# Optimization experiments

Measured on AMD Instinct MI355X. Metric: run time of the kernel, lower is better.

Reference implementation:

```python
import jax, jax.numpy as jnp
import numpy as np

D_LATENT, D_HIDDEN, D_TIME, K = 128, 256, 16, 3
B, NX = 8, 4096
MSG_IN = 2 * D_LATENT + 1 + D_TIME + 2  # 275
UPD_IN = 2 * D_LATENT + D_TIME          # 272


def _gelu(v):
    return jax.nn.gelu(v, approximate=False)  # torch nn.GELU default (erf)


def _linear_params(key, din, dout):
    k1, k2 = jax.random.split(key)
    bound = 1.0 / np.sqrt(din)
    w = jax.random.uniform(k1, (din, dout), minval=-bound, maxval=bound, dtype=jnp.float32)
    b = jax.random.uniform(k2, (dout,), minval=-bound, maxval=bound, dtype=jnp.float32)
    return w, b


def setup_inputs() -> dict:
    key = jax.random.key(0)
    ks = jax.random.split(key, 16)
    inp = {
        'h': jax.random.normal(ks[0], (B, NX, D_LATENT), dtype=jnp.float32),
        'x': jax.random.uniform(ks[1], (B, NX), dtype=jnp.float32),
        'tau': jax.random.normal(ks[2], (B, D_TIME), dtype=jnp.float32),
        'u0': jax.random.normal(ks[3], (B, NX), dtype=jnp.float32),
    }
    inp['msg_w1'], inp['msg_b1'] = _linear_params(ks[4], MSG_IN, D_HIDDEN)
    inp['msg_w2'], inp['msg_b2'] = _linear_params(ks[5], D_HIDDEN, D_HIDDEN)
    inp['msg_w3'], inp['msg_b3'] = _linear_params(ks[6], D_HIDDEN, D_LATENT)
    inp['gate_w1'], inp['gate_b1'] = _linear_params(ks[7], MSG_IN, D_HIDDEN)
    inp['gate_w2'], inp['gate_b2'] = _linear_params(ks[8], D_HIDDEN, 1)
    inp['upd_w1'], inp['upd_b1'] = _linear_params(ks[9], UPD_IN, D_HIDDEN)
    inp['upd_w2'], inp['upd_b2'] = _linear_params(ks[10], D_HIDDEN, D_HIDDEN)
    inp['upd_w3'], inp['upd_b3'] = _linear_params(ks[11], D_HIDDEN, D_LATENT)
    inp['W_w'], inp['W_b'] = _linear_params(ks[12], D_LATENT, D_LATENT)
    return inp


def reference(h, x, tau, u0, msg_w1, msg_b1, msg_w2, msg_b2, msg_w3, msg_b3,
              gate_w1, gate_b1, gate_w2, gate_b2,
              upd_w1, upd_b1, upd_w2, upd_b2, upd_w3, upd_b3, W_w, W_b):
    Bq, nx, d = h.shape
    k = K
    S = 2 * k + 1
    # replicate padding along the spatial dim
    h_pad = jnp.pad(h, ((0, 0), (k, k), (0, 0)), mode='edge')
    x_pad = jnp.pad(x, ((0, 0), (k, k)), mode='edge')
    u0_pad = jnp.pad(u0, ((0, 0), (k, k)), mode='edge')
    # all stencil windows at once: idx[nx, S] gathers neighbor j for node i
    idx = jnp.arange(nx)[:, None] + jnp.arange(S)[None, :]
    h_j = h_pad[:, idx, :]                                  # [B, nx, S, d]
    rel = (x_pad[:, idx] - x[:, :, None])[..., None]        # [B, nx, S, 1]
    du0 = (u0[:, :, None] - u0_pad[:, idx])[..., None]      # [B, nx, S, 1]
    h_e = jnp.broadcast_to(h[:, :, None, :], (Bq, nx, S, d))
    tau_e = jnp.broadcast_to(tau[:, None, None, :], (Bq, nx, S, tau.shape[-1]))
    msg_in = jnp.concatenate([h_e, h_j, rel, tau_e, du0, jnp.abs(du0)], axis=-1)  # [B,nx,S,275]
    a = _gelu(msg_in @ msg_w1 + msg_b1)
    a = _gelu(a @ msg_w2 + msg_b2)
    msg = a @ msg_w3 + msg_b3                               # [B, nx, S, d]
    g = _gelu(msg_in @ gate_w1 + gate_b1)
    gate = jax.nn.sigmoid(g @ gate_w2 + gate_b2)            # [B, nx, S, 1]
    agg = jnp.sum(gate * msg, axis=2)                       # [B, nx, d]
    tau_n = jnp.broadcast_to(tau[:, None, :], (Bq, nx, tau.shape[-1]))
    upd_in = jnp.concatenate([h, agg, tau_n], axis=-1)      # [B, nx, 272]
    u = _gelu(upd_in @ upd_w1 + upd_b1)
    u = _gelu(u @ upd_w2 + upd_b2)
    h_nonlocal = u @ upd_w3 + upd_b3
    h_local = h @ W_w + W_b
    return _gelu(h_nonlocal + h_local)
```

## Files before the change

kernel.cpp:

```cpp
#include <hip/hip_runtime.h>
#include <hip/hip_bf16.h>
#include <math.h>

#define NXC 4096
#define NNODES 32768

typedef __attribute__((ext_vector_type(8))) short bf16x8;
typedef __attribute__((ext_vector_type(4))) short s16x4;
typedef __attribute__((ext_vector_type(16))) float f32x16;

#define MFMA32(a,b,c) __builtin_amdgcn_mfma_f32_32x32x16_bf16((a),(b),(c),0,0,0)

__device__ __forceinline__ float gelu_f(float v) {
    float z = v * fmaf(v*v, 0.10294324f, 2.3022082f);
    float e = __builtin_amdgcn_exp2f(z);
    return v - v * __builtin_amdgcn_rcpf(1.0f + e);
}
__device__ __forceinline__ float sigmoid_f(float v) {
    float e = __builtin_amdgcn_exp2f(-1.4426950409f * v);
    return __builtin_amdgcn_rcpf(1.0f + e);
}
__device__ __forceinline__ short f2bs(float x) {
    __hip_bfloat16 b = __float2bfloat16(x);
    union { __hip_bfloat16 h; short s; } u; u.h = b; return u.s;
}
__device__ __forceinline__ f32x16 zero16() {
    f32x16 v;
    #pragma unroll
    for (int i = 0; i < 16; ++i) v[i] = 0.f;
    return v;
}
__device__ __forceinline__ float dpp_xor1(float x) {
    return __int_as_float(__builtin_amdgcn_update_dpp(0, __float_as_int(x), 0xB1, 0xF, 0xF, true));
}
__device__ __forceinline__ float dpp_xor2(float x) {
    return __int_as_float(__builtin_amdgcn_update_dpp(0, __float_as_int(x), 0x4E, 0xF, 0xF, true));
}

__global__ void tau_kernel(const float* __restrict__ tau,
                           const float* __restrict__ msg_w1, const float* __restrict__ msg_b1,
                           const float* __restrict__ gate_w1, const float* __restrict__ gate_b1,
                           const float* __restrict__ upd_w1, const float* __restrict__ upd_b1,
                           float* __restrict__ TM, float* __restrict__ TG, float* __restrict__ TU)
{
    const int b = blockIdx.x;
    const int t = threadIdx.x;
    float tv[16];
    #pragma unroll
    for (int k = 0; k < 16; ++k) tv[k] = tau[b*16 + k];
    float am = msg_b1[t], ag = gate_b1[t], au = upd_b1[t];
    #pragma unroll
    for (int k = 0; k < 16; ++k) {
        am = fmaf(tv[k], msg_w1 [(257+k)*256 + t], am);
        ag = fmaf(tv[k], gate_w1[(257+k)*256 + t], ag);
        au = fmaf(tv[k], upd_w1 [(256+k)*256 + t], au);
    }
    TM[b*256+t] = am; TG[b*256+t] = ag; TU[b*256+t] = au;
}

__global__ void wconv_kernel(const float* __restrict__ msg_w2, const float* __restrict__ msg_w3,
                             const float* __restrict__ msg_w1, const float* __restrict__ gate_w1,
                             const float* __restrict__ upd_w1, const float* __restrict__ upd_w2,
                             const float* __restrict__ upd_w3, const float* __restrict__ W_w,
                             __hip_bfloat16* __restrict__ w2t, __hip_bfloat16* __restrict__ w3t,
                             __hip_bfloat16* __restrict__ wall_t, __hip_bfloat16* __restrict__ w1ut,
                             __hip_bfloat16* __restrict__ w2ut, __hip_bfloat16* __restrict__ w3ut,
                             __hip_bfloat16* __restrict__ wwt)
{
    int i = blockIdx.x * 256 + threadIdx.x;
    if (i < 65536) { int c=i>>8, k=i&255; w2t[i] = __float2bfloat16(msg_w2[k*256+c]); return; }
    i -= 65536;
    if (i < 32768) { int c=i>>8, k=i&255; w3t[i] = __float2bfloat16(msg_w3[k*128+c]); return; }
    i -= 32768;
    if (i < 131072) {
        int c = i>>7, k = i&127; float v;
        if      (c <  256) v = msg_w1 [k*256 + c];
        else if (c <  512) v = msg_w1 [(128+k)*256 + (c-256)];
        else if (c <  768) v = gate_w1[k*256 + (c-512)];
        else               v = gate_w1[(128+k)*256 + (c-768)];
        wall_t[i] = __float2bfloat16(v); return;
    }
    i -= 131072;
    if (i < 65536) { int c=i>>8, k=i&255; w1ut[i] = __float2bfloat16(upd_w1[k*256+c]); return; }
    i -= 65536;
    if (i < 65536) { int c=i>>8, k=i&255; w2ut[i] = __float2bfloat16(upd_w2[k*256+c]); return; }
    i -= 65536;
    if (i < 32768) { int c=i>>8, k=i&255; w3ut[i] = __float2bfloat16(upd_w3[k*128+c]); return; }
    i -= 32768;
    { int c=i>>7, k=i&127; wwt[i] = __float2bfloat16(W_w[k*128+c]); }
}

#define PSTR 136

__global__ __launch_bounds__(256, 4)
void precompute_kernel(const float* __restrict__ h, const __hip_bfloat16* __restrict__ wall_t,
                       __hip_bfloat16* __restrict__ PAm, __hip_bfloat16* __restrict__ PBm,
                       __hip_bfloat16* __restrict__ PAg, __hip_bfloat16* __restrict__ PBg)
{
    __shared__ __align__(16) __hip_bfloat16 lds[64*256];
    const int t = threadIdx.x;
    const int lane = t & 63, wv = t >> 6;
    const int cl = lane & 31, g = lane >> 5;
    const int base = blockIdx.x * 64;
    const int tile = blockIdx.y;

    #pragma unroll
    for (int i = 0; i < 8; ++i) {
        int f = (i*256 + t)*4;
        float4 hv = *(const float4*)&h[(size_t)base*128 + f];
        int row = f >> 7, col = f & 127;
        s16x4 pk; pk[0]=f2bs(hv.x); pk[1]=f2bs(hv.y); pk[2]=f2bs(hv.z); pk[3]=f2bs(hv.w);
        *(s16x4*)&lds[row*PSTR + col] = pk;
    }
    __syncthreads();

    f32x16 a00 = zero16(), a01 = zero16(), a10 = zero16(), a11 = zero16();
    {
        const int c0 = wv*64 + cl, c1 = c0 + 32;
        const __hip_bfloat16* b0 = wall_t + ((size_t)tile*256 + c0)*128 + g*8;
        const __hip_bfloat16* b1 = wall_t + ((size_t)tile*256 + c1)*128 + g*8;
        const __hip_bfloat16* a0 = lds + (size_t)(cl)*PSTR + g*8;
        const __hip_bfloat16* a1p = lds + (size_t)(32+cl)*PSTR + g*8;
        #pragma unroll
        for (int kt = 0; kt < 8; ++kt) {
            bf16x8 bf0 = *(const bf16x8*)(b0 + kt*16);
            bf16x8 bf1 = *(const bf16x8*)(b1 + kt*16);
            bf16x8 af0 = *(const bf16x8*)(a0 + kt*16);
            bf16x8 af1 = *(const bf16x8*)(a1p + kt*16);
            a00 = MFMA32(af0, bf0, a00);
            a01 = MFMA32(af0, bf1, a01);
            a10 = MFMA32(af1, bf0, a10);
            a11 = MFMA32(af1, bf1, a11);
        }
    }
    __syncthreads();
    {
        const int c0 = wv*64 + cl, c1 = c0 + 32;
        #pragma unroll
        for (int r = 0; r < 16; ++r) {
            int row = (r&3) + 8*(r>>2) + 4*g;
            lds[row*256 + c0]      = __float2bfloat16(a00[r]);
            lds[row*256 + c1]      = __float2bfloat16(a01[r]);
            lds[(32+row)*256 + c0] = __float2bfloat16(a10[r]);
            lds[(32+row)*256 + c1] = __float2bfloat16(a11[r]);
        }
    }
    __syncthreads();
    {
        __hip_bfloat16* bufs[4] = {PAm, PBm, PAg, PBg};
        __hip_bfloat16* dst = bufs[tile];
        #pragma unroll
        for (int i = 0; i < 8; ++i) {
            int idx = i*256 + t;
            int row = idx >> 5, ch = idx & 31;
            *(float4*)&dst[(size_t)(base+row)*256 + ch*8] =
                *(const float4*)&lds[row*256 + ch*8];
        }
    }
}

#define ENPB 8
#define EEPB 56
#define ARS  264
#define MRS  132

__global__ __launch_bounds__(256, 4)
void edge_kernel(const float* __restrict__ x, const float* __restrict__ u0,
                 const float* __restrict__ msg_w1, const float* __restrict__ gate_w1,
                 const __hip_bfloat16* __restrict__ w2t, const float* __restrict__ msg_b2,
                 const __hip_bfloat16* __restrict__ w3t, const float* __restrict__ msg_b3,
                 const float* __restrict__ gate_w2, const float* __restrict__ gate_b2,
                 const __hip_bfloat16* __restrict__ PAm, const __hip_bfloat16* __restrict__ PBm,
                 const __hip_bfloat16* __restrict__ PAg, const __hip_bfloat16* __restrict__ PBg,
                 const float* __restrict__ TM, const float* __restrict__ TG,
                 float* __restrict__ AGG)
{
    __shared__ __align__(16) __hip_bfloat16 act[64*ARS];
    __shared__ float s_gp[4][EEPB];
    __shared__ float s_rel[EEPB], s_du[EEPB], s_ad[EEPB];
    __shared__ int   s_slotj[14];
    __shared__ float s_gate[EEPB];

    const int t    = threadIdx.x;
    const int lane = t & 63;
    const int wv   = t >> 6;
    const int base = blockIdx.x * ENPB;
    const int b    = base >> 12;
    const int ii0  = base & (NXC-1);

    if (t < 14) {
        int jj = ii0 - 3 + t;
        jj = jj < 0 ? 0 : (jj > NXC-1 ? NXC-1 : jj);
        s_slotj[t] = b*NXC + jj;
    }
    if (t < EEPB) {
        int nd = t / 7, s = t - nd*7;
        int i  = base + nd;
        int jj = ii0 + nd + s - 3;
        jj = jj < 0 ? 0 : (jj > NXC-1 ? NXC-1 : jj);
        int j = b*NXC + jj;
        float rel = x[j] - x[i];
        float du  = u0[i] - u0[j];
        s_rel[t] = rel; s_du[t] = du; s_ad[t] = fabsf(du);
    }
    __syncthreads();

    {
        float wr  = msg_w1 [256*256+t], wd  = msg_w1 [273*256+t], wa  = msg_w1 [274*256+t];
        float gwr = gate_w1[256*256+t], gwd = gate_w1[273*256+t], gwa = gate_w1[274*256+t];
        float tm = TM[b*256+t], tg = TG[b*256+t];
        float g2 = gate_w2[t];
        float bm[14], bg[14], pam[8], pag[8], sacc[14];
        #pragma unroll
        for (int q = 0; q < 14; ++q) {
            size_t o = (size_t)s_slotj[q]*256 + t;
            bm[q] = __bfloat162float(PBm[o]) + tm;
            bg[q] = __bfloat162float(PBg[o]) + tg;
        }
        #pragma unroll
        for (int nd = 0; nd < 8; ++nd) {
            size_t o = (size_t)(base+nd)*256 + t;
            pam[nd] = __bfloat162float(PAm[o]);
            pag[nd] = __bfloat162float(PAg[o]);
        }
        const bool p1 = (lane & 1), p2 = ((lane & 2) != 0);
        #pragma unroll
        for (int m = 0; m < 14; ++m) {
            float gq[4];
            #pragma unroll
            for (int r4i = 0; r4i < 4; ++r4i) {
                const int e = m*4 + r4i;
                const int nd = e / 7, s = e - nd*7, q = nd + s;
                float rel = s_rel[e], du = s_du[e], ad = s_ad[e];
                float pm = pam[nd] + bm[q];
                pm = fmaf(rel, wr, pm); pm = fmaf(du, wd, pm); pm = fmaf(ad, wa, pm);
                act[e*ARS + t] = __float2bfloat16(gelu_f(pm));
                float pg = pag[nd] + bg[q];
                pg = fmaf(rel, gwr, pg); pg = fmaf(du, gwd, pg); pg = fmaf(ad, gwa, pg);
                gq[r4i] = gelu_f(pg) * g2;
            }
            float xx = p1 ? gq[1] : gq[0], yy = p1 ? gq[0] : gq[1];
            xx += dpp_xor1(yy);
            float zz = p1 ? gq[3] : gq[2], ww = p1 ? gq[2] : gq[3];
            zz += dpp_xor1(ww);
            float uu = p2 ? zz : xx, vv = p2 ? xx : zz;
            uu += dpp_xor2(vv);
            sacc[m] = uu;
        }
        #pragma unroll
        for (int m = 0; m < 14; ++m) {
            float v = sacc[m];
            v += __shfl_xor(v, 4);
            v += __shfl_xor(v, 8);
            v += __shfl_xor(v, 16);
            v += __shfl_xor(v, 32);
            if (lane < 4) s_gp[wv][m*4 + lane] = v;
        }
    }
    __syncthreads();
    if (t < EEPB)
        s_gate[t] = sigmoid_f(s_gp[0][t] + s_gp[1][t] + s_gp[2][t] + s_gp[3][t] + gate_b2[0]);

    const int cl = lane & 31;
    const int g  = lane >> 5;
    f32x16 acc00 = zero16(), acc01 = zero16(), acc10 = zero16(), acc11 = zero16();
    {
        const __hip_bfloat16* w2a = w2t + (size_t)((wv*2+0)*32 + cl)*256 + g*8;
        const __hip_bfloat16* w2b = w2t + (size_t)((wv*2+1)*32 + cl)*256 + g*8;
        const __hip_bfloat16* a1a = act + (size_t)(cl)*ARS + g*8;
        const __hip_bfloat16* a1b = act + (size_t)(32+cl)*ARS + g*8;
        #pragma unroll
        for (int kt = 0; kt < 16; ++kt) {
            bf16x8 bfa = *(const bf16x8*)(w2a + kt*16);
            bf16x8 bfb = *(const bf16x8*)(w2b + kt*16);
            bf16x8 afa = *(const bf16x8*)(a1a + kt*16);
            bf16x8 afb = *(const bf16x8*)(a1b + kt*16);
            acc00 = MFMA32(afa, bfa, acc00);
            acc01 = MFMA32(afa, bfb, acc01);
            acc10 = MFMA32(afb, bfa, acc10);
            acc11 = MFMA32(afb, bfb, acc11);
        }
    }
    __syncthreads();
    {
        const int c0 = (wv*2+0)*32 + cl;
        const int c1 = (wv*2+1)*32 + cl;
        float b20 = msg_b2[c0], b21 = msg_b2[c1];
        #pragma unroll
        for (int r = 0; r < 16; ++r) {
            int row0 = (r&3) + 8*(r>>2) + 4*g;
            act[row0*ARS + c0] = __float2bfloat16(gelu_f(acc00[r] + b20));
            act[row0*ARS + c1] = __float2bfloat16(gelu_f(acc01[r] + b21));
            if (r < 12) {
                int row1 = 32 + row0;
                act[row1*ARS + c0] = __float2bfloat16(gelu_f(acc10[r] + b20));
                act[row1*ARS + c1] = __float2bfloat16(gelu_f(acc11[r] + b21));
            }
        }
    }
    __syncthreads();

    f32x16 m0 = zero16(), m1 = zero16();
    {
        const __hip_bfloat16* w3p = w3t + (size_t)(wv*32 + cl)*256 + g*8;
        const __hip_bfloat16* a2a = act + (size_t)(cl)*ARS + g*8;
        const __hip_bfloat16* a2b = act + (size_t)(32+cl)*ARS + g*8;
        #pragma unroll
        for (int kt = 0; kt < 16; ++kt) {
            bf16x8 bfr = *(const bf16x8*)(w3p + kt*16);
            m0 = MFMA32(*(const bf16x8*)(a2a + kt*16), bfr, m0);
            m1 = MFMA32(*(const bf16x8*)(a2b + kt*16), bfr, m1);
        }
    }
    __syncthreads();
    float* msgbuf = (float*)act;
    {
        const int c = wv*32 + cl;
        float b3v = msg_b3[c];
        #pragma unroll
        for (int r = 0; r < 16; ++r) {
            int row0 = (r&3) + 8*(r>>2) + 4*g;
            int row1 = 32 + row0;
            msgbuf[row0*MRS + c] = (m0[r] + b3v) * s_gate[row0];
            if (row1 < EEPB)
                msgbuf[row1*MRS + c] = (m1[r] + b3v) * s_gate[row1];
        }
    }
    __syncthreads();

    {
        const int c   = t & 127;
        const int grp = t >> 7;
        #pragma unroll
        for (int p = 0; p < 4; ++p) {
            int nd = grp + p*2;
            float ssum = 0.f;
            #pragma unroll
            for (int q2 = 0; q2 < 7; ++q2) ssum += msgbuf[(nd*7+q2)*MRS + c];
            AGG[(size_t)(base+nd)*128 + c] = ssum;
        }
    }
}

#define UM 32

__global__ __launch_bounds__(256, 4)
void update_kernel(const __hip_bfloat16* __restrict__ w1ut, const __hip_bfloat16* __restrict__ w2ut,
                   const __hip_bfloat16* __restrict__ w3ut, const __hip_bfloat16* __restrict__ wwt,
                   const float* __restrict__ upd_b2, const float* __restrict__ upd_b3,
                   const float* __restrict__ W_b,
                   const float* __restrict__ h, const float* __restrict__ AGG,
                   const float* __restrict__ TU,
                   float* __restrict__ out)
{
    __shared__ __align__(16) __hip_bfloat16 ub[UM*ARS];
    const int t = threadIdx.x;
    const int lane = t & 63, wv = t >> 6;
    const int cl = lane & 31, g = lane >> 5;
    const int base = blockIdx.x * UM;
    const int b = base >> 12;

    #pragma unroll
    for (int i = 0; i < 4; ++i) {
        int f = (i*256 + t)*4;
        int row = f >> 7, col = f & 127;
        float4 hv = *(const float4*)&h[(size_t)base*128 + f];
        s16x4 pk; pk[0]=f2bs(hv.x); pk[1]=f2bs(hv.y); pk[2]=f2bs(hv.z); pk[3]=f2bs(hv.w);
        *(s16x4*)&ub[row*ARS + col] = pk;
        float4 av = *(const float4*)&AGG[(size_t)base*128 + f];
        s16x4 pa; pa[0]=f2bs(av.x); pa[1]=f2bs(av.y); pa[2]=f2bs(av.z); pa[3]=f2bs(av.w);
        *(s16x4*)&ub[row*ARS + 128 + col] = pa;
    }
    __syncthreads();

    f32x16 u0a = zero16(), u1a = zero16(), hl = zero16();
    {
        const __hip_bfloat16* a0 = ub + (size_t)(cl)*ARS + g*8;
        const __hip_bfloat16* b0 = w1ut + (size_t)(wv*64 + cl)*256 + g*8;
        const __hip_bfloat16* b1 = w1ut + (size_t)(wv*64 + 32 + cl)*256 + g*8;
        const __hip_bfloat16* bw = wwt + (size_t)(wv*32 + cl)*128 + g*8;
        #pragma unroll
        for (int kt = 0; kt < 16; ++kt) {
            bf16x8 af = *(const bf16x8*)(a0 + kt*16);
            u0a = MFMA32(af, *(const bf16x8*)(b0 + kt*16), u0a);
            u1a = MFMA32(af, *(const bf16x8*)(b1 + kt*16), u1a);
            if (kt < 8)
                hl = MFMA32(af, *(const bf16x8*)(bw + kt*16), hl);
        }
    }
    __syncthreads();
    {
        const int c0 = wv*64 + cl, c1 = c0 + 32;
        float tu0 = TU[b*256 + c0], tu1 = TU[b*256 + c1];
        #pragma unroll
        for (int r = 0; r < 16; ++r) {
            int row = (r&3) + 8*(r>>2) + 4*g;
            ub[row*ARS + c0] = __float2bfloat16(gelu_f(u0a[r] + tu0));
            ub[row*ARS + c1] = __float2bfloat16(gelu_f(u1a[r] + tu1));
        }
    }
    __syncthreads();

    f32x16 v0a = zero16(), v1a = zero16();
    {
        const __hip_bfloat16* a0 = ub + (size_t)(cl)*ARS + g*8;
        const __hip_bfloat16* b0 = w2ut + (size_t)(wv*64 + cl)*256 + g*8;
        const __hip_bfloat16* b1 = w2ut + (size_t)(wv*64 + 32 + cl)*256 + g*8;
        #pragma unroll
        for (int kt = 0; kt < 16; ++kt) {
            bf16x8 af = *(const bf16x8*)(a0 + kt*16);
            v0a = MFMA32(af, *(const bf16x8*)(b0 + kt*16), v0a);
            v1a = MFMA32(af, *(const bf16x8*)(b1 + kt*16), v1a);
        }
    }
    __syncthreads();
    {
        const int c0 = wv*64 + cl, c1 = c0 + 32;
        float b20 = upd_b2[c0], b21 = upd_b2[c1];
        #pragma unroll
        for (int r = 0; r < 16; ++r) {
            int row = (r&3) + 8*(r>>2) + 4*g;
            ub[row*ARS + c0] = __float2bfloat16(gelu_f(v0a[r] + b20));
            ub[row*ARS + c1] = __float2bfloat16(gelu_f(v1a[r] + b21));
        }
    }
    __syncthreads();

    f32x16 w0a = zero16();
    {
        const __hip_bfloat16* wp = w3ut + (size_t)(wv*32 + cl)*256 + g*8;
        const __hip_bfloat16* a0 = ub + (size_t)(cl)*ARS + g*8;
        #pragma unroll
        for (int kt = 0; kt < 16; ++kt)
            w0a = MFMA32(*(const bf16x8*)(a0 + kt*16), *(const bf16x8*)(wp + kt*16), w0a);
    }
    {
        const int c = wv*32 + cl;
        float b3v = upd_b3[c] + W_b[c];
        #pragma unroll
        for (int r = 0; r < 16; ++r) {
            int row = (r&3) + 8*(r>>2) + 4*g;
            size_t o = (size_t)(base+row)*128 + c;
            out[o] = gelu_f(w0a[r] + b3v + hl[r]);
        }
    }
}

extern "C" void kernel_launch(void* const* d_in, const int* in_sizes, int n_in,
                              void* d_out, int out_size, void* d_ws, size_t ws_size,
                              hipStream_t stream)
{
    const float* h      = (const float*)d_in[0];
    const float* x      = (const float*)d_in[1];
    const float* tau    = (const float*)d_in[2];
    const float* u0     = (const float*)d_in[3];
    const float* msg_w1 = (const float*)d_in[4];
    const float* msg_b1 = (const float*)d_in[5];
    const float* msg_w2 = (const float*)d_in[6];
    const float* msg_b2 = (const float*)d_in[7];
    const float* msg_w3 = (const float*)d_in[8];
    const float* msg_b3 = (const float*)d_in[9];
    const float* gate_w1= (const float*)d_in[10];
    const float* gate_b1= (const float*)d_in[11];
    const float* gate_w2= (const float*)d_in[12];
    const float* gate_b2= (const float*)d_in[13];
    const float* upd_w1 = (const float*)d_in[14];
    const float* upd_b1 = (const float*)d_in[15];
    const float* upd_w2 = (const float*)d_in[16];
    const float* upd_b2 = (const float*)d_in[17];
    const float* upd_w3 = (const float*)d_in[18];
    const float* upd_b3 = (const float*)d_in[19];
    const float* W_w    = (const float*)d_in[20];
    const float* W_b    = (const float*)d_in[21];
    float* out = (float*)d_out;

    char* ws = (char*)d_ws;
    size_t off = 0;
    auto alloc = [&](size_t bytes) -> void* {
        void* p = ws + off;
        off += (bytes + 255) & ~(size_t)255;
        return p;
    };
    __hip_bfloat16* PAm = (__hip_bfloat16*)alloc((size_t)NNODES*256*2);
    __hip_bfloat16* PBm = (__hip_bfloat16*)alloc((size_t)NNODES*256*2);
    __hip_bfloat16* PAg = (__hip_bfloat16*)alloc((size_t)NNODES*256*2);
    __hip_bfloat16* PBg = (__hip_bfloat16*)alloc((size_t)NNODES*256*2);
    float* AGG = (float*)alloc((size_t)NNODES*128*4);
    float* TM  = (float*)alloc(8*256*4);
    float* TG  = (float*)alloc(8*256*4);
    float* TU  = (float*)alloc(8*256*4);
    __hip_bfloat16* w2t   = (__hip_bfloat16*)alloc((size_t)256*256*2);
    __hip_bfloat16* w3t   = (__hip_bfloat16*)alloc((size_t)128*256*2);
    __hip_bfloat16* wall_t= (__hip_bfloat16*)alloc((size_t)1024*128*2);
    __hip_bfloat16* w1ut  = (__hip_bfloat16*)alloc((size_t)256*256*2);
    __hip_bfloat16* w2ut  = (__hip_bfloat16*)alloc((size_t)256*256*2);
    __hip_bfloat16* w3ut  = (__hip_bfloat16*)alloc((size_t)128*256*2);
    __hip_bfloat16* wwt   = (__hip_bfloat16*)alloc((size_t)128*128*2);
    (void)ws_size; (void)in_sizes; (void)n_in; (void)out_size;

    tau_kernel<<<8, 256, 0, stream>>>(tau, msg_w1, msg_b1, gate_w1, gate_b1,
                                      upd_w1, upd_b1, TM, TG, TU);
    wconv_kernel<<<1600, 256, 0, stream>>>(msg_w2, msg_w3, msg_w1, gate_w1,
                                           upd_w1, upd_w2, upd_w3, W_w,
                                           w2t, w3t, wall_t, w1ut, w2ut, w3ut, wwt);
    precompute_kernel<<<dim3(NNODES/64, 4), 256, 0, stream>>>(h, wall_t,
                                                              PAm, PBm, PAg, PBg);
    edge_kernel<<<NNODES/ENPB, 256, 0, stream>>>(x, u0, msg_w1, gate_w1,
                                                 w2t, msg_b2, w3t, msg_b3,
                                                 gate_w2, gate_b2,
                                                 PAm, PBm, PAg, PBg, TM, TG, AGG);
    update_kernel<<<NNODES/UM, 256, 0, stream>>>(w1ut, w2ut, w3ut, wwt,
                                                 upd_b2, upd_b3, W_b,
                                                 h, AGG, TU, out);
}
```

Baseline: 205.0 us.

## Fuse tau into wconv, loop precompute tiles, pack GELU pairs, store AGG in bf16

Folds the tau projection kernel into the weight-conversion kernel as extra blocks, which removes one launch. The precompute kernel now loads h once per block and loops over all four output tiles, instead of using a 2D grid that reloads h for each tile. GELU and the elementwise math in the edge and update kernels are rewritten on 2-wide float vectors to allow packed FP32 instructions. AGG is stored as bf16, which halves its traffic and makes the update kernel's load a plain copy, at some precision cost in the intermediate. The trade-offs are fewer precompute blocks with more LDS each and extra barriers inside the tile loop.

```diff
diff --git a/kernel.cpp b/kernel.cpp
--- a/kernel.cpp
+++ b/kernel.cpp
@@ -8,6 +8,7 @@
 typedef __attribute__((ext_vector_type(8))) short bf16x8;
 typedef __attribute__((ext_vector_type(4))) short s16x4;
 typedef __attribute__((ext_vector_type(16))) float f32x16;
+typedef __attribute__((ext_vector_type(2))) float f32x2;
 
 #define MFMA32(a,b,c) __builtin_amdgcn_mfma_f32_32x32x16_bf16((a),(b),(c),0,0,0)
 
@@ -15,6 +16,15 @@
     float z = v * fmaf(v*v, 0.10294324f, 2.3022082f);
     float e = __builtin_amdgcn_exp2f(z);
     return v - v * __builtin_amdgcn_rcpf(1.0f + e);
+}
+__device__ __forceinline__ f32x2 gelu2(f32x2 v) {
+    const f32x2 c1 = {0.10294324f, 0.10294324f};
+    const f32x2 c2 = {2.3022082f, 2.3022082f};
+    f32x2 z = v * __builtin_elementwise_fma(v*v, c1, c2);
+    f32x2 r;
+    r[0] = __builtin_amdgcn_rcpf(1.0f + __builtin_amdgcn_exp2f(z[0]));
+    r[1] = __builtin_amdgcn_rcpf(1.0f + __builtin_amdgcn_exp2f(z[1]));
+    return v - v * r;
 }
 __device__ __forceinline__ float sigmoid_f(float v) {
     float e = __builtin_amdgcn_exp2f(-1.4426950409f * v);
@@ -37,36 +47,35 @@
     return __int_as_float(__builtin_amdgcn_update_dpp(0, __float_as_int(x), 0x4E, 0xF, 0xF, true));
 }
 
-__global__ void tau_kernel(const float* __restrict__ tau,
-                           const float* __restrict__ msg_w1, const float* __restrict__ msg_b1,
-                           const float* __restrict__ gate_w1, const float* __restrict__ gate_b1,
-                           const float* __restrict__ upd_w1, const float* __restrict__ upd_b1,
-                           float* __restrict__ TM, float* __restrict__ TG, float* __restrict__ TU)
-{
-    const int b = blockIdx.x;
-    const int t = threadIdx.x;
-    float tv[16];
-    #pragma unroll
-    for (int k = 0; k < 16; ++k) tv[k] = tau[b*16 + k];
-    float am = msg_b1[t], ag = gate_b1[t], au = upd_b1[t];
-    #pragma unroll
-    for (int k = 0; k < 16; ++k) {
-        am = fmaf(tv[k], msg_w1 [(257+k)*256 + t], am);
-        ag = fmaf(tv[k], gate_w1[(257+k)*256 + t], ag);
-        au = fmaf(tv[k], upd_w1 [(256+k)*256 + t], au);
-    }
-    TM[b*256+t] = am; TG[b*256+t] = ag; TU[b*256+t] = au;
-}
-
 __global__ void wconv_kernel(const float* __restrict__ msg_w2, const float* __restrict__ msg_w3,
                              const float* __restrict__ msg_w1, const float* __restrict__ gate_w1,
                              const float* __restrict__ upd_w1, const float* __restrict__ upd_w2,
                              const float* __restrict__ upd_w3, const float* __restrict__ W_w,
+                             const float* __restrict__ tau,
+                             const float* __restrict__ msg_b1, const float* __restrict__ gate_b1,
+                             const float* __restrict__ upd_b1,
                              __hip_bfloat16* __restrict__ w2t, __hip_bfloat16* __restrict__ w3t,
                              __hip_bfloat16* __restrict__ wall_t, __hip_bfloat16* __restrict__ w1ut,
                              __hip_bfloat16* __restrict__ w2ut, __hip_bfloat16* __restrict__ w3ut,
-                             __hip_bfloat16* __restrict__ wwt)
+                             __hip_bfloat16* __restrict__ wwt,
+                             float* __restrict__ TM, float* __restrict__ TG, float* __restrict__ TU)
 {
+    if (blockIdx.x >= 1600) {
+        const int b = blockIdx.x - 1600;
+        const int t = threadIdx.x;
+        float tv[16];
+        #pragma unroll
+        for (int k = 0; k < 16; ++k) tv[k] = tau[b*16 + k];
+        float am = msg_b1[t], ag = gate_b1[t], au = upd_b1[t];
+        #pragma unroll
+        for (int k = 0; k < 16; ++k) {
+            am = fmaf(tv[k], msg_w1 [(257+k)*256 + t], am);
+            ag = fmaf(tv[k], gate_w1[(257+k)*256 + t], ag);
+            au = fmaf(tv[k], upd_w1 [(256+k)*256 + t], au);
+        }
+        TM[b*256+t] = am; TG[b*256+t] = ag; TU[b*256+t] = au;
+        return;
+    }
     int i = blockIdx.x * 256 + threadIdx.x;
     if (i < 65536) { int c=i>>8, k=i&255; w2t[i] = __float2bfloat16(msg_w2[k*256+c]); return; }
     i -= 65536;
@@ -92,17 +101,17 @@
 
 #define PSTR 136
 
-__global__ __launch_bounds__(256, 4)
+__global__ __launch_bounds__(256, 3)
 void precompute_kernel(const float* __restrict__ h, const __hip_bfloat16* __restrict__ wall_t,
                        __hip_bfloat16* __restrict__ PAm, __hip_bfloat16* __restrict__ PBm,
                        __hip_bfloat16* __restrict__ PAg, __hip_bfloat16* __restrict__ PBg)
 {
-    __shared__ __align__(16) __hip_bfloat16 lds[64*256];
+    __shared__ __align__(16) __hip_bfloat16 hs[64*PSTR];
+    __shared__ __align__(16) __hip_bfloat16 ob[64*256];
     const int t = threadIdx.x;
     const int lane = t & 63, wv = t >> 6;
     const int cl = lane & 31, g = lane >> 5;
     const int base = blockIdx.x * 64;
-    const int tile = blockIdx.y;
 
     #pragma unroll
     for (int i = 0; i < 8; ++i) {
@@ -110,52 +119,50 @@
         float4 hv = *(const float4*)&h[(size_t)base*128 + f];
         int row = f >> 7, col = f & 127;
         s16x4 pk; pk[0]=f2bs(hv.x); pk[1]=f2bs(hv.y); pk[2]=f2bs(hv.z); pk[3]=f2bs(hv.w);
-        *(s16x4*)&lds[row*PSTR + col] = pk;
-    }
-    __syncthreads();
-
-    f32x16 a00 = zero16(), a01 = zero16(), a10 = zero16(), a11 = zero16();
-    {
-        const int c0 = wv*64 + cl, c1 = c0 + 32;
-        const __hip_bfloat16* b0 = wall_t + ((size_t)tile*256 + c0)*128 + g*8;
-        const __hip_bfloat16* b1 = wall_t + ((size_t)tile*256 + c1)*128 + g*8;
-        const __hip_bfloat16* a0 = lds + (size_t)(cl)*PSTR + g*8;
-        const __hip_bfloat16* a1p = lds + (size_t)(32+cl)*PSTR + g*8;
-        #pragma unroll
-        for (int kt = 0; kt < 8; ++kt) {
-            bf16x8 bf0 = *(const bf16x8*)(b0 + kt*16);
-            bf16x8 bf1 = *(const bf16x8*)(b1 + kt*16);
-            bf16x8 af0 = *(const bf16x8*)(a0 + kt*16);
-            bf16x8 af1 = *(const bf16x8*)(a1p + kt*16);
-            a00 = MFMA32(af0, bf0, a00);
-            a01 = MFMA32(af0, bf1, a01);
-            a10 = MFMA32(af1, bf0, a10);
-            a11 = MFMA32(af1, bf1, a11);
-        }
-    }
-    __syncthreads();
-    {
-        const int c0 = wv*64 + cl, c1 = c0 + 32;
+        *(s16x4*)&hs[row*PSTR + col] = pk;
+    }
+    __syncthreads();
+
+    __hip_bfloat16* bufs[4] = {PAm, PBm, PAg, PBg};
+    const int c0 = wv*64 + cl, c1 = c0 + 32;
+    const __hip_bfloat16* a0  = hs + (size_t)(cl)*PSTR + g*8;
+    const __hip_bfloat16* a1p = hs + (size_t)(32+cl)*PSTR + g*8;
+
+    for (int tile = 0; tile < 4; ++tile) {
+        f32x16 a00 = zero16(), a01 = zero16(), a10 = zero16(), a11 = zero16();
+        {
+            const __hip_bfloat16* b0 = wall_t + ((size_t)tile*256 + c0)*128 + g*8;
+            const __hip_bfloat16* b1 = wall_t + ((size_t)tile*256 + c1)*128 + g*8;
+            #pragma unroll
+            for (int kt = 0; kt < 8; ++kt) {
+                bf16x8 bf0 = *(const bf16x8*)(b0 + kt*16);
+                bf16x8 bf1 = *(const bf16x8*)(b1 + kt*16);
+                bf16x8 af0 = *(const bf16x8*)(a0 + kt*16);
+                bf16x8 af1 = *(const bf16x8*)(a1p + kt*16);
+                a00 = MFMA32(af0, bf0, a00);
+                a01 = MFMA32(af0, bf1, a01);
+                a10 = MFMA32(af1, bf0, a10);
+                a11 = MFMA32(af1, bf1, a11);
+            }
+        }
         #pragma unroll
         for (int r = 0; r < 16; ++r) {
             int row = (r&3) + 8*(r>>2) + 4*g;
-            lds[row*256 + c0]      = __float2bfloat16(a00[r]);
-            lds[row*256 + c1]      = __float2bfloat16(a01[r]);
-            lds[(32+row)*256 + c0] = __float2bfloat16(a10[r]);
-            lds[(32+row)*256 + c1] = __float2bfloat16(a11[r]);
-        }
-    }
-    __syncthreads();
-    {
-        __hip_bfloat16* bufs[4] = {PAm, PBm, PAg, PBg};
+            ob[row*256 + c0]      = __float2bfloat16(a00[r]);
+            ob[row*256 + c1]      = __float2bfloat16(a01[r]);
+            ob[(32+row)*256 + c0] = __float2bfloat16(a10[r]);
+            ob[(32+row)*256 + c1] = __float2bfloat16(a11[r]);
+        }
+        __syncthreads();
         __hip_bfloat16* dst = bufs[tile];
         #pragma unroll
         for (int i = 0; i < 8; ++i) {
             int idx = i*256 + t;
             int row = idx >> 5, ch = idx & 31;
             *(float4*)&dst[(size_t)(base+row)*256 + ch*8] =
-                *(const float4*)&lds[row*256 + ch*8];
-        }
+                *(const float4*)&ob[row*256 + ch*8];
+        }
+        __syncthreads();
     }
 }
 
@@ -173,11 +180,11 @@
                  const __hip_bfloat16* __restrict__ PAm, const __hip_bfloat16* __restrict__ PBm,
                  const __hip_bfloat16* __restrict__ PAg, const __hip_bfloat16* __restrict__ PBg,
                  const float* __restrict__ TM, const float* __restrict__ TG,
-                 float* __restrict__ AGG)
+                 __hip_bfloat16* __restrict__ AGG)
 {
     __shared__ __align__(16) __hip_bfloat16 act[64*ARS];
+    __shared__ __align__(16) float s_rel[EEPB], s_du[EEPB], s_ad[EEPB];
     __shared__ float s_gp[4][EEPB];
-    __shared__ float s_rel[EEPB], s_du[EEPB], s_ad[EEPB];
     __shared__ int   s_slotj[14];
     __shared__ float s_gate[EEPB];
 
@@ -210,6 +217,9 @@
         float gwr = gate_w1[256*256+t], gwd = gate_w1[273*256+t], gwa = gate_w1[274*256+t];
         float tm = TM[b*256+t], tg = TG[b*256+t];
         float g2 = gate_w2[t];
+        const f32x2 wr2  = {wr, wr},  wd2  = {wd, wd},  wa2  = {wa, wa};
+        const f32x2 gwr2 = {gwr,gwr}, gwd2 = {gwd,gwd}, gwa2 = {gwa,gwa};
+        const f32x2 g22  = {g2, g2};
         float bm[14], bg[14], pam[8], pag[8], sacc[14];
         #pragma unroll
         for (int q = 0; q < 14; ++q) {
@@ -225,19 +235,29 @@
         }
         const bool p1 = (lane & 1), p2 = ((lane & 2) != 0);
         #pragma unroll
-        for (int m = 0; m < 14; ++m) {
+        for (int mq = 0; mq < 14; ++mq) {
             float gq[4];
             #pragma unroll
-            for (int r4i = 0; r4i < 4; ++r4i) {
-                const int e = m*4 + r4i;
-                const int nd = e / 7, s = e - nd*7, q = nd + s;
-                float rel = s_rel[e], du = s_du[e], ad = s_ad[e];
-                float pm = pam[nd] + bm[q];
-                pm = fmaf(rel, wr, pm); pm = fmaf(du, wd, pm); pm = fmaf(ad, wa, pm);
-                act[e*ARS + t] = __float2bfloat16(gelu_f(pm));
-                float pg = pag[nd] + bg[q];
-                pg = fmaf(rel, gwr, pg); pg = fmaf(du, gwd, pg); pg = fmaf(ad, gwa, pg);
-                gq[r4i] = gelu_f(pg) * g2;
+            for (int pp = 0; pp < 2; ++pp) {
+                const int e0 = mq*4 + pp*2, e1 = e0 + 1;
+                const int nd0 = e0/7, q0 = nd0 + (e0 - nd0*7);
+                const int nd1 = e1/7, q1 = nd1 + (e1 - nd1*7);
+                f32x2 rel = *(const f32x2*)&s_rel[e0];
+                f32x2 du  = *(const f32x2*)&s_du[e0];
+                f32x2 ad  = *(const f32x2*)&s_ad[e0];
+                f32x2 pm; pm[0] = pam[nd0] + bm[q0]; pm[1] = pam[nd1] + bm[q1];
+                pm = __builtin_elementwise_fma(rel, wr2, pm);
+                pm = __builtin_elementwise_fma(du,  wd2, pm);
+                pm = __builtin_elementwise_fma(ad,  wa2, pm);
+                f32x2 gm = gelu2(pm);
+                act[e0*ARS + t] = __float2bfloat16(gm[0]);
+                act[e1*ARS + t] = __float2bfloat16(gm[1]);
+                f32x2 pg; pg[0] = pag[nd0] + bg[q0]; pg[1] = pag[nd1] + bg[q1];
+                pg = __builtin_elementwise_fma(rel, gwr2, pg);
+                pg = __builtin_elementwise_fma(du,  gwd2, pg);
+                pg = __builtin_elementwise_fma(ad,  gwa2, pg);
+                f32x2 gg = gelu2(pg) * g22;
+                gq[pp*2] = gg[0]; gq[pp*2+1] = gg[1];
             }
             float xx = p1 ? gq[1] : gq[0], yy = p1 ? gq[0] : gq[1];
             xx += dpp_xor1(yy);
@@ -245,7 +265,7 @@
             zz += dpp_xor1(ww);
             float uu = p2 ? zz : xx, vv = p2 ? xx : zz;
             uu += dpp_xor2(vv);
-            sacc[m] = uu;
+            sacc[mq] = uu;
         }
         #pragma unroll
         for (int m = 0; m < 14; ++m) {
@@ -287,14 +307,26 @@
         const int c1 = (wv*2+1)*32 + cl;
         float b20 = msg_b2[c0], b21 = msg_b2[c1];
         #pragma unroll
-        for (int r = 0; r < 16; ++r) {
+        for (int r = 0; r < 16; r += 2) {
             int row0 = (r&3) + 8*(r>>2) + 4*g;
-            act[row0*ARS + c0] = __float2bfloat16(gelu_f(acc00[r] + b20));
-            act[row0*ARS + c1] = __float2bfloat16(gelu_f(acc01[r] + b21));
+            f32x2 v0 = {acc00[r] + b20, acc00[r+1] + b20};
+            f32x2 g0 = gelu2(v0);
+            act[row0*ARS + c0]     = __float2bfloat16(g0[0]);
+            act[(row0+1)*ARS + c0] = __float2bfloat16(g0[1]);
+            f32x2 v1 = {acc01[r] + b21, acc01[r+1] + b21};
+            f32x2 g1 = gelu2(v1);
+            act[row0*ARS + c1]     = __float2bfloat16(g1[0]);
+            act[(row0+1)*ARS + c1] = __float2bfloat16(g1[1]);
             if (r < 12) {
                 int row1 = 32 + row0;
-                act[row1*ARS + c0] = __float2bfloat16(gelu_f(acc10[r] + b20));
-                act[row1*ARS + c1] = __float2bfloat16(gelu_f(acc11[r] + b21));
+                f32x2 v2 = {acc10[r] + b20, acc10[r+1] + b20};
+                f32x2 g2v = gelu2(v2);
+                act[row1*ARS + c0]     = __float2bfloat16(g2v[0]);
+                act[(row1+1)*ARS + c0] = __float2bfloat16(g2v[1]);
+                f32x2 v3 = {acc11[r] + b21, acc11[r+1] + b21};
+                f32x2 g3 = gelu2(v3);
+                act[row1*ARS + c1]     = __float2bfloat16(g3[0]);
+                act[(row1+1)*ARS + c1] = __float2bfloat16(g3[1]);
             }
         }
     }
@@ -318,26 +350,39 @@
         const int c = wv*32 + cl;
         float b3v = msg_b3[c];
         #pragma unroll
-        for (int r = 0; r < 16; ++r) {
+        for (int r = 0; r < 16; r += 2) {
             int row0 = (r&3) + 8*(r>>2) + 4*g;
+            f32x2 mm = {m0[r] + b3v, m0[r+1] + b3v};
+            f32x2 gt = {s_gate[row0], s_gate[row0+1]};
+            mm *= gt;
+            msgbuf[row0*MRS + c]     = mm[0];
+            msgbuf[(row0+1)*MRS + c] = mm[1];
             int row1 = 32 + row0;
-            msgbuf[row0*MRS + c] = (m0[r] + b3v) * s_gate[row0];
-            if (row1 < EEPB)
-                msgbuf[row1*MRS + c] = (m1[r] + b3v) * s_gate[row1];
-        }
-    }
-    __syncthreads();
-
-    {
-        const int c   = t & 127;
-        const int grp = t >> 7;
-        #pragma unroll
-        for (int p = 0; p < 4; ++p) {
-            int nd = grp + p*2;
-            float ssum = 0.f;
+            if (row1 + 1 < EEPB) {
+                f32x2 nn = {m1[r] + b3v, m1[r+1] + b3v};
+                f32x2 ht = {s_gate[row1], s_gate[row1+1]};
+                nn *= ht;
+                msgbuf[row1*MRS + c]     = nn[0];
+                msgbuf[(row1+1)*MRS + c] = nn[1];
+            }
+        }
+    }
+    __syncthreads();
+
+    {
+        const int c2  = (t & 63) * 2;
+        const int grp = t >> 6;
+        #pragma unroll
+        for (int p = 0; p < 2; ++p) {
+            int nd = grp + p*4;
+            f32x2 s = {0.f, 0.f};
             #pragma unroll
-            for (int q2 = 0; q2 < 7; ++q2) ssum += msgbuf[(nd*7+q2)*MRS + c];
-            AGG[(size_t)(base+nd)*128 + c] = ssum;
+            for (int q2 = 0; q2 < 7; ++q2)
+                s += *(const f32x2*)&msgbuf[(nd*7+q2)*MRS + c2];
+            ushort2 u;
+            u.x = (unsigned short)f2bs(s[0]);
+            u.y = (unsigned short)f2bs(s[1]);
+            *(ushort2*)&AGG[(size_t)(base+nd)*128 + c2] = u;
         }
     }
 }
@@ -349,7 +394,7 @@
                    const __hip_bfloat16* __restrict__ w3ut, const __hip_bfloat16* __restrict__ wwt,
                    const float* __restrict__ upd_b2, const float* __restrict__ upd_b3,
                    const float* __restrict__ W_b,
-                   const float* __restrict__ h, const float* __restrict__ AGG,
+                   const float* __restrict__ h, const __hip_bfloat16* __restrict__ AGG,
                    const float* __restrict__ TU,
                    float* __restrict__ out)
 {
@@ -367,9 +412,13 @@
         float4 hv = *(const float4*)&h[(size_t)base*128 + f];
         s16x4 pk; pk[0]=f2bs(hv.x); pk[1]=f2bs(hv.y); pk[2]=f2bs(hv.z); pk[3]=f2bs(hv.w);
         *(s16x4*)&ub[row*ARS + col] = pk;
-        float4 av = *(const float4*)&AGG[(size_t)base*128 + f];
-        s16x4 pa; pa[0]=f2bs(av.x); pa[1]=f2bs(av.y); pa[2]=f2bs(av.z); pa[3]=f2bs(av.w);
-        *(s16x4*)&ub[row*ARS + 128 + col] = pa;
+    }
+    #pragma unroll
+    for (int i = 0; i < 2; ++i) {
+        int idx = i*256 + t;
+        int row = idx >> 4, ch = idx & 15;
+        *(float4*)&ub[row*ARS + 128 + ch*8] =
+            *(const float4*)&AGG[(size_t)(base+row)*128 + ch*8];
     }
     __syncthreads();
 
@@ -393,10 +442,16 @@
         const int c0 = wv*64 + cl, c1 = c0 + 32;
         float tu0 = TU[b*256 + c0], tu1 = TU[b*256 + c1];
         #pragma unroll
-        for (int r = 0; r < 16; ++r) {
+        for (int r = 0; r < 16; r += 2) {
             int row = (r&3) + 8*(r>>2) + 4*g;
-            ub[row*ARS + c0] = __float2bfloat16(gelu_f(u0a[r] + tu0));
-            ub[row*ARS + c1] = __float2bfloat16(gelu_f(u1a[r] + tu1));
+            f32x2 v0 = {u0a[r] + tu0, u0a[r+1] + tu0};
+            f32x2 g0 = gelu2(v0);
+            ub[row*ARS + c0]     = __float2bfloat16(g0[0]);
+            ub[(row+1)*ARS + c0] = __float2bfloat16(g0[1]);
+            f32x2 v1 = {u1a[r] + tu1, u1a[r+1] + tu1};
+            f32x2 g1 = gelu2(v1);
+            ub[row*ARS + c1]     = __float2bfloat16(g1[0]);
+            ub[(row+1)*ARS + c1] = __float2bfloat16(g1[1]);
         }
     }
     __syncthreads();
@@ -418,10 +473,16 @@
         const int c0 = wv*64 + cl, c1 = c0 + 32;
         float b20 = upd_b2[c0], b21 = upd_b2[c1];
         #pragma unroll
-        for (int r = 0; r < 16; ++r) {
+        for (int r = 0; r < 16; r += 2) {
             int row = (r&3) + 8*(r>>2) + 4*g;
-            ub[row*ARS + c0] = __float2bfloat16(gelu_f(v0a[r] + b20));
-            ub[row*ARS + c1] = __float2bfloat16(gelu_f(v1a[r] + b21));
+            f32x2 v0 = {v0a[r] + b20, v0a[r+1] + b20};
+            f32x2 g0 = gelu2(v0);
+            ub[row*ARS + c0]     = __float2bfloat16(g0[0]);
+            ub[(row+1)*ARS + c0] = __float2bfloat16(g0[1]);
+            f32x2 v1 = {v1a[r] + b21, v1a[r+1] + b21};
+            f32x2 g1 = gelu2(v1);
+            ub[row*ARS + c1]     = __float2bfloat16(g1[0]);
+            ub[(row+1)*ARS + c1] = __float2bfloat16(g1[1]);
         }
     }
     __syncthreads();
@@ -485,7 +546,7 @@
     __hip_bfloat16* PBm = (__hip_bfloat16*)alloc((size_t)NNODES*256*2);
     __hip_bfloat16* PAg = (__hip_bfloat16*)alloc((size_t)NNODES*256*2);
     __hip_bfloat16* PBg = (__hip_bfloat16*)alloc((size_t)NNODES*256*2);
-    float* AGG = (float*)alloc((size_t)NNODES*128*4);
+    __hip_bfloat16* AGG = (__hip_bfloat16*)alloc((size_t)NNODES*128*2);
     float* TM  = (float*)alloc(8*256*4);
     float* TG  = (float*)alloc(8*256*4);
     float* TU  = (float*)alloc(8*256*4);
@@ -498,13 +559,13 @@
     __hip_bfloat16* wwt   = (__hip_bfloat16*)alloc((size_t)128*128*2);
     (void)ws_size; (void)in_sizes; (void)n_in; (void)out_size;
 
-    tau_kernel<<<8, 256, 0, stream>>>(tau, msg_w1, msg_b1, gate_w1, gate_b1,
-                                      upd_w1, upd_b1, TM, TG, TU);
-    wconv_kernel<<<1600, 256, 0, stream>>>(msg_w2, msg_w3, msg_w1, gate_w1,
+    wconv_kernel<<<1608, 256, 0, stream>>>(msg_w2, msg_w3, msg_w1, gate_w1,
                                            upd_w1, upd_w2, upd_w3, W_w,
-                                           w2t, w3t, wall_t, w1ut, w2ut, w3ut, wwt);
-    precompute_kernel<<<dim3(NNODES/64, 4), 256, 0, stream>>>(h, wall_t,
-                                                              PAm, PBm, PAg, PBg);
+                                           tau, msg_b1, gate_b1, upd_b1,
+                                           w2t, w3t, wall_t, w1ut, w2ut, w3ut, wwt,
+                                           TM, TG, TU);
+    precompute_kernel<<<NNODES/64, 256, 0, stream>>>(h, wall_t,
+                                                     PAm, PBm, PAg, PBg);
     edge_kernel<<<NNODES/ENPB, 256, 0, stream>>>(x, u0, msg_w1, gate_w1,
                                                  w2t, msg_b2, w3t, msg_b3,
                                                  gate_w2, gate_b2,
```

New measurement: 200.4 us. -2.2%, faster.
